# Kernel optimization log

Measured on AMD Instinct MI355X. Metric: run time of the kernel, lower is better.

## Reference

```python
import jax, jax.numpy as jnp
import numpy as np

MARGIN = 0.3

def setup_inputs() -> dict:
    key = jax.random.key(0)
    k1, k2 = jax.random.split(key)
    z1 = jax.random.normal(k1, (8192, 128), dtype=jnp.float32)
    z2 = jax.random.normal(k2, (8192, 128), dtype=jnp.float32)
    return {"z1": z1, "z2": z2}

def _cdist(z1, z2):
    # Euclidean pairwise distances via the GEMM identity, avoiding the
    # [N, N, d] broadcasted intermediate. Clamp for numerical safety.
    sq1 = jnp.sum(z1 * z1, axis=1, keepdims=True)        # [N, 1]
    sq2 = jnp.sum(z2 * z2, axis=1, keepdims=True).T      # [1, N]
    d2 = sq1 + sq2 - 2.0 * (z1 @ z2.T)                   # [N, N]
    return jnp.sqrt(jnp.maximum(d2, 0.0))

def reference(z1, z2) -> jnp.ndarray:
    n = z1.shape[0]
    dist = _cdist(z1, z2)                                # [N, N]
    pos_dist = jnp.diagonal(dist)                        # [N]
    # hard negative mining: mask diagonal with +inf, take row-min
    eye = jnp.eye(n, dtype=bool)
    neg_dist = jnp.where(eye, jnp.inf, dist)
    hard_neg = jnp.min(neg_dist, axis=1)                 # [N]
    loss = jax.nn.relu(pos_dist - hard_neg + MARGIN)
    return jnp.mean(loss)
```

## Files before the change

kernel.cpp:

```cpp
#include <hip/hip_runtime.h>

#define MARGIN 0.3f

typedef __attribute__((ext_vector_type(8))) short short8;
typedef __attribute__((ext_vector_type(4))) float floatx4;


__device__ __forceinline__ unsigned enc_f32(float f) {
    unsigned u = __float_as_uint(f);
    return (u & 0x80000000u) ? ~u : (u | 0x80000000u);
}
__device__ __forceinline__ float dec_f32(unsigned u) {
    return (u & 0x80000000u) ? __uint_as_float(u & 0x7fffffffu)
                             : __uint_as_float(~u);
}
__device__ __forceinline__ short f2bf(float f) {
    unsigned u = __float_as_uint(f);
    u = u + 0x7fffu + ((u >> 16) & 1u);
    return (short)(u >> 16);
}

__device__ __forceinline__ void gload_lds16(const void* g, void* l) {
    __builtin_amdgcn_global_load_lds(
        (const __attribute__((address_space(1))) void*)g,
        (__attribute__((address_space(3))) void*)l, 16, 0, 0);
}
__device__ __forceinline__ void gload_lds4(const void* g, void* l) {
    __builtin_amdgcn_global_load_lds(
        (const __attribute__((address_space(1))) void*)g,
        (__attribute__((address_space(3))) void*)l, 4, 0, 0);
}


__global__ void prep_kernel(const float* __restrict__ z1, const float* __restrict__ z2,
                            short* __restrict__ z1b, short* __restrict__ z2b,
                            float* __restrict__ sq1, float* __restrict__ sq2,
                            float* __restrict__ posd, unsigned* __restrict__ rowmin,
                            unsigned* __restrict__ cnt, float* __restrict__ out) {
    int h = blockIdx.x * 256 + threadIdx.x;
    int row = h >> 4, p = h & 15;
    int kk = p >> 2, q = p & 3;
    int f0 = row * 32 + kk * 8 + q * 2;
    float4 fa0 = ((const float4*)z1)[f0], fa1 = ((const float4*)z1)[f0 + 1];
    float4 fb0 = ((const float4*)z2)[f0], fb1 = ((const float4*)z2)[f0 + 1];
    short8 sa = { f2bf(fa0.x), f2bf(fa0.y), f2bf(fa0.z), f2bf(fa0.w),
                  f2bf(fa1.x), f2bf(fa1.y), f2bf(fa1.z), f2bf(fa1.w) };
    short8 sb = { f2bf(fb0.x), f2bf(fb0.y), f2bf(fb0.z), f2bf(fb0.w),
                  f2bf(fb1.x), f2bf(fb1.y), f2bf(fb1.z), f2bf(fb1.w) };
    size_t off = (size_t)(row >> 4) * 2048 + kk * 512 + q * 128 + (row & 15) * 8;
    *(short8*)&z1b[off] = sa;
    *(short8*)&z2b[off] = sb;

    float s1 = fa0.x*fa0.x + fa0.y*fa0.y + fa0.z*fa0.z + fa0.w*fa0.w
             + fa1.x*fa1.x + fa1.y*fa1.y + fa1.z*fa1.z + fa1.w*fa1.w;
    float s2 = fb0.x*fb0.x + fb0.y*fb0.y + fb0.z*fb0.z + fb0.w*fb0.w
             + fb1.x*fb1.x + fb1.y*fb1.y + fb1.z*fb1.z + fb1.w*fb1.w;
    float dx0 = fa0.x-fb0.x, dy0 = fa0.y-fb0.y, dz0 = fa0.z-fb0.z, dw0 = fa0.w-fb0.w;
    float dx1 = fa1.x-fb1.x, dy1 = fa1.y-fb1.y, dz1 = fa1.z-fb1.z, dw1 = fa1.w-fb1.w;
    float p2 = dx0*dx0 + dy0*dy0 + dz0*dz0 + dw0*dw0
             + dx1*dx1 + dy1*dy1 + dz1*dz1 + dw1*dw1;
    #pragma unroll
    for (int m = 8; m >= 1; m >>= 1) {
        s1 += __shfl_xor(s1, m);
        s2 += __shfl_xor(s2, m);
        p2 += __shfl_xor(p2, m);
    }
    if (p == 0) { sq1[row] = s1; sq2[row] = s2; posd[row] = sqrtf(p2); }

    if (threadIdx.x < 16) rowmin[blockIdx.x * 16 + threadIdx.x] = 0xFFFFFFFFu;
    if (blockIdx.x == 0) {
        if (threadIdx.x < 32) cnt[threadIdx.x] = 0u;
        if (threadIdx.x == 0) out[0] = 0.0f;
    }
}

__global__ __launch_bounds__(512, 2)
void gemm_min_kernel(const short* __restrict__ z1b, const short* __restrict__ z2b,
                     const float* __restrict__ sq1, const float* __restrict__ sq2,
                     const float* __restrict__ posd,
                     unsigned* __restrict__ rowmin, unsigned* __restrict__ cnt,
                     float* __restrict__ out, int n)
{
    __shared__ __align__(16) short sb[8][8192];
    __shared__ __align__(16) float s2l[512];
    __shared__ float lsum[8];
    __shared__ int   fin_s;

    const int bid = blockIdx.x;
    const int xcd = bid & 7, idx = bid >> 3;
    const int rg  = (xcd << 1) | (idx >> 4);
    const int cgi = idx & 15;

    const int tid = threadIdx.x, w = tid >> 6, lane = tid & 63;
    const int quad = lane >> 4, l15 = lane & 15;
    const int rowbase = rg * 512 + w * 64;
    const int colorig = cgi * 512;

    const short* gb = z2b + (size_t)(cgi * 32) * 2048;

    #pragma unroll
    for (int o = 0; o < 2; ++o)
        gload_lds16(gb + (tid + o * 512) * 8, &sb[0][(tid + o * 512) * 8]);
    __builtin_amdgcn_sched_barrier(0);
    gload_lds4(sq2 + colorig + tid, &s2l[tid]);
    __builtin_amdgcn_sched_barrier(0);

    short8 af[4][4];
    #pragma unroll
    for (int sm = 0; sm < 4; ++sm) {
        const short* pa = z1b + (size_t)(rg * 32 + w * 4 + sm) * 2048 + lane * 8;
        #pragma unroll
        for (int kk = 0; kk < 4; ++kk)
            af[sm][kk] = *(const short8*)(pa + kk * 512);
    }
    __builtin_amdgcn_sched_barrier(0);
    #pragma unroll
    for (int s = 1; s < 8; ++s) {
        #pragma unroll
        for (int o = 0; o < 2; ++o)
            gload_lds16(gb + (size_t)s * 8192 + (tid + o * 512) * 8,
                        &sb[s][(tid + o * 512) * 8]);
        __builtin_amdgcn_sched_barrier(0);
    }

    float vmin[4][4];
    #pragma unroll
    for (int sm = 0; sm < 4; ++sm)
        #pragma unroll
        for (int reg = 0; reg < 4; ++reg)
            vmin[sm][reg] = 3.0e38f;

#define SUPERPHASE(S, VMTXT)                                                   \
    do {                                                                       \
        asm volatile("s_waitcnt vmcnt(" VMTXT ")" ::: "memory");               \
        __builtin_amdgcn_sched_barrier(0);                                     \
        __builtin_amdgcn_s_barrier();                                          \
        __builtin_amdgcn_sched_barrier(0);                                     \
        const short* bs_ = &sb[S][0];                                          \
        _Pragma("unroll")                                                      \
        for (int hf = 0; hf < 2; ++hf) {                                       \
            const int tcol = (S) * 64 + hf * 32;                               \
            const int colbase = colorig + tcol;                                \
            const float s2v0 = s2l[tcol + l15];                                \
            const float s2v1 = s2l[tcol + 16 + l15];                           \
            short8 bq[2][4];                                                   \
            _Pragma("unroll")                                                  \
            for (int sn = 0; sn < 2; ++sn)                                     \
                _Pragma("unroll")                                              \
                for (int kk = 0; kk < 4; ++kk)                                 \
                    bq[sn][kk] = *(const short8*)(bs_ + hf * 4096 + sn * 2048  \
                                                  + kk * 512 + lane * 8);      \
            floatx4 acc[4][2];                                                 \
            _Pragma("unroll")                                                  \
            for (int sm = 0; sm < 4; ++sm)                                     \
                _Pragma("unroll")                                              \
                for (int sn = 0; sn < 2; ++sn)                                 \
                    acc[sm][sn] = (floatx4)0.0f;                               \
            _Pragma("unroll")                                                  \
            for (int kk = 0; kk < 4; ++kk)                                     \
                _Pragma("unroll")                                              \
                for (int sm = 0; sm < 4; ++sm)                                 \
                    _Pragma("unroll")                                          \
                    for (int sn = 0; sn < 2; ++sn)                             \
                        acc[sm][sn] = __builtin_amdgcn_mfma_f32_16x16x32_bf16( \
                            af[sm][kk], bq[sn][kk], acc[sm][sn], 0, 0, 0);     \
            if (colbase < rowbase + 64 && rowbase < colbase + 32) {            \
                _Pragma("unroll")                                              \
                for (int sm = 0; sm < 4; ++sm)                                 \
                    _Pragma("unroll")                                          \
                    for (int reg = 0; reg < 4; ++reg) {                        \
                        int gi = rowbase + sm * 16 + quad * 4 + reg;           \
                        float v0 = fmaf(-2.0f, acc[sm][0][reg], s2v0);         \
                        float v1 = fmaf(-2.0f, acc[sm][1][reg], s2v1);         \
                        v0 = (gi == colbase + l15)      ? 3.0e38f : v0;        \
                        v1 = (gi == colbase + 16 + l15) ? 3.0e38f : v1;        \
                        vmin[sm][reg] = fminf(vmin[sm][reg], fminf(v0, v1));   \
                    }                                                          \
            } else {                                                           \
                _Pragma("unroll")                                              \
                for (int sm = 0; sm < 4; ++sm)                                 \
                    _Pragma("unroll")                                          \
                    for (int reg = 0; reg < 4; ++reg) {                        \
                        float v0 = fmaf(-2.0f, acc[sm][0][reg], s2v0);         \
                        float v1 = fmaf(-2.0f, acc[sm][1][reg], s2v1);         \
                        vmin[sm][reg] = fminf(vmin[sm][reg], fminf(v0, v1));   \
                    }                                                          \
            }                                                                  \
        }                                                                      \
    } while (0)

    SUPERPHASE(0, "14");
    SUPERPHASE(1, "12");
    SUPERPHASE(2, "10");
    SUPERPHASE(3, "8");
    SUPERPHASE(4, "6");
    SUPERPHASE(5, "4");
    SUPERPHASE(6, "2");
    SUPERPHASE(7, "0");
#undef SUPERPHASE

    #pragma unroll
    for (int sm = 0; sm < 4; ++sm)
        #pragma unroll
        for (int reg = 0; reg < 4; ++reg) {
            float vm = vmin[sm][reg];
            #pragma unroll
            for (int m = 8; m >= 1; m >>= 1)
                vm = fminf(vm, __shfl_xor(vm, m));
            if (l15 == 0)
                atomicMin(&rowmin[rowbase + sm * 16 + quad * 4 + reg], enc_f32(vm));
        }

    __syncthreads();
    if (tid == 0) {
        __threadfence();
        fin_s = (atomicAdd(&cnt[rg], 1u) == 15u);
    }
    __syncthreads();
    if (!fin_s) return;
    __threadfence();

    {
        int i = rg * 512 + tid;
        unsigned rm = atomicMin(&rowmin[i], 0xFFFFFFFFu);
        float hard = sqrtf(fmaxf(sq1[i] + dec_f32(rm), 0.0f));
        float l = fmaxf(posd[i] - hard + MARGIN, 0.0f);
        #pragma unroll
        for (int m = 32; m >= 1; m >>= 1) l += __shfl_xor(l, m);
        if (lane == 0) lsum[w] = l;
    }
    __syncthreads();
    if (tid == 0) {
        float t = 0.f;
        #pragma unroll
        for (int i = 0; i < 8; ++i) t += lsum[i];
        atomicAdd(out, t / (float)n);
    }
}

extern "C" void kernel_launch(void* const* d_in, const int* in_sizes, int n_in,
                              void* d_out, int out_size, void* d_ws, size_t ws_size,
                              hipStream_t stream) {
    const float* z1 = (const float*)d_in[0];
    const float* z2 = (const float*)d_in[1];
    const int n = in_sizes[0] / 128;

    char* ws = (char*)d_ws;
    short*    z1b    = (short*)ws;
    short*    z2b    = (short*)(ws + (size_t)n * 128 * 2);
    float*    sq1    = (float*)(ws + (size_t)n * 128 * 4);
    float*    sq2    = (float*)(ws + (size_t)n * 128 * 4 + n * 4);
    float*    posd   = (float*)(ws + (size_t)n * 128 * 4 + n * 8);
    unsigned* rowmin = (unsigned*)(ws + (size_t)n * 128 * 4 + n * 12);
    unsigned* cnt    = (unsigned*)(ws + (size_t)n * 128 * 4 + n * 16);
    float*    out    = (float*)d_out;

    prep_kernel<<<n / 16, 256, 0, stream>>>(z1, z2, z1b, z2b, sq1, sq2, posd,
                                            rowmin, cnt, out);
    gemm_min_kernel<<<(n / 512) * (n / 512), 512, 0, stream>>>(
        z1b, z2b, sq1, sq2, posd, rowmin, cnt, out, n);
}
```

Measured before the change: 84.02 us.

## Fold -2 scale into bf16 z2 and seed MFMA accumulators with sq2

The prep kernel now stores z2 pre-scaled by -2 in bf16, and the GEMM accumulators are initialised with the column squared norms. The MFMA output is therefore already sq2 - 2·dot, which removes the per-element fma from the min epilogue. The change also raises wave priority around the MFMA block with s_setprio and switches the prep kernel's stores to nontemporal. Multiplying by -2 before bf16 rounding is exact, so precision is unchanged, but accumulator setup now costs register moves instead of zero initialisation.

```diff
diff --git a/kernel.cpp b/kernel.cpp
--- a/kernel.cpp
+++ b/kernel.cpp
@@ -45,11 +45,11 @@
     float4 fb0 = ((const float4*)z2)[f0], fb1 = ((const float4*)z2)[f0 + 1];
     short8 sa = { f2bf(fa0.x), f2bf(fa0.y), f2bf(fa0.z), f2bf(fa0.w),
                   f2bf(fa1.x), f2bf(fa1.y), f2bf(fa1.z), f2bf(fa1.w) };
-    short8 sb = { f2bf(fb0.x), f2bf(fb0.y), f2bf(fb0.z), f2bf(fb0.w),
-                  f2bf(fb1.x), f2bf(fb1.y), f2bf(fb1.z), f2bf(fb1.w) };
+    short8 sb = { f2bf(-2.f*fb0.x), f2bf(-2.f*fb0.y), f2bf(-2.f*fb0.z), f2bf(-2.f*fb0.w),
+                  f2bf(-2.f*fb1.x), f2bf(-2.f*fb1.y), f2bf(-2.f*fb1.z), f2bf(-2.f*fb1.w) };
     size_t off = (size_t)(row >> 4) * 2048 + kk * 512 + q * 128 + (row & 15) * 8;
-    *(short8*)&z1b[off] = sa;
-    *(short8*)&z2b[off] = sb;
+    __builtin_nontemporal_store(sa, (short8*)&z1b[off]);
+    __builtin_nontemporal_store(sb, (short8*)&z2b[off]);
 
     float s1 = fa0.x*fa0.x + fa0.y*fa0.y + fa0.z*fa0.z + fa0.w*fa0.w
              + fa1.x*fa1.x + fa1.y*fa1.y + fa1.z*fa1.z + fa1.w*fa1.w;
@@ -65,9 +65,14 @@
         s2 += __shfl_xor(s2, m);
         p2 += __shfl_xor(p2, m);
     }
-    if (p == 0) { sq1[row] = s1; sq2[row] = s2; posd[row] = sqrtf(p2); }
-
-    if (threadIdx.x < 16) rowmin[blockIdx.x * 16 + threadIdx.x] = 0xFFFFFFFFu;
+    if (p == 0) {
+        __builtin_nontemporal_store(s1, &sq1[row]);
+        __builtin_nontemporal_store(s2, &sq2[row]);
+        __builtin_nontemporal_store(sqrtf(p2), &posd[row]);
+    }
+
+    if (threadIdx.x < 16)
+        __builtin_nontemporal_store(0xFFFFFFFFu, &rowmin[blockIdx.x * 16 + threadIdx.x]);
     if (blockIdx.x == 0) {
         if (threadIdx.x < 32) cnt[threadIdx.x] = 0u;
         if (threadIdx.x == 0) out[0] = 0.0f;
@@ -152,10 +157,14 @@
                                                   + kk * 512 + lane * 8);      \
             floatx4 acc[4][2];                                                 \
             _Pragma("unroll")                                                  \
-            for (int sm = 0; sm < 4; ++sm)                                     \
-                _Pragma("unroll")                                              \
-                for (int sn = 0; sn < 2; ++sn)                                 \
-                    acc[sm][sn] = (floatx4)0.0f;                               \
+            for (int sm = 0; sm < 4; ++sm) {                                   \
+                _Pragma("unroll")                                              \
+                for (int reg = 0; reg < 4; ++reg) {                            \
+                    acc[sm][0][reg] = s2v0;                                    \
+                    acc[sm][1][reg] = s2v1;                                    \
+                }                                                              \
+            }                                                                  \
+            __builtin_amdgcn_s_setprio(1);                                     \
             _Pragma("unroll")                                                  \
             for (int kk = 0; kk < 4; ++kk)                                     \
                 _Pragma("unroll")                                              \
@@ -164,14 +173,15 @@
                     for (int sn = 0; sn < 2; ++sn)                             \
                         acc[sm][sn] = __builtin_amdgcn_mfma_f32_16x16x32_bf16( \
                             af[sm][kk], bq[sn][kk], acc[sm][sn], 0, 0, 0);     \
+            __builtin_amdgcn_s_setprio(0);                                     \
             if (colbase < rowbase + 64 && rowbase < colbase + 32) {            \
                 _Pragma("unroll")                                              \
                 for (int sm = 0; sm < 4; ++sm)                                 \
                     _Pragma("unroll")                                          \
                     for (int reg = 0; reg < 4; ++reg) {                        \
                         int gi = rowbase + sm * 16 + quad * 4 + reg;           \
-                        float v0 = fmaf(-2.0f, acc[sm][0][reg], s2v0);         \
-                        float v1 = fmaf(-2.0f, acc[sm][1][reg], s2v1);         \
+                        float v0 = acc[sm][0][reg];                            \
+                        float v1 = acc[sm][1][reg];                            \
                         v0 = (gi == colbase + l15)      ? 3.0e38f : v0;        \
                         v1 = (gi == colbase + 16 + l15) ? 3.0e38f : v1;        \
                         vmin[sm][reg] = fminf(vmin[sm][reg], fminf(v0, v1));   \
@@ -180,11 +190,9 @@
                 _Pragma("unroll")                                              \
                 for (int sm = 0; sm < 4; ++sm)                                 \
                     _Pragma("unroll")                                          \
-                    for (int reg = 0; reg < 4; ++reg) {                        \
-                        float v0 = fmaf(-2.0f, acc[sm][0][reg], s2v0);         \
-                        float v1 = fmaf(-2.0f, acc[sm][1][reg], s2v1);         \
-                        vmin[sm][reg] = fminf(vmin[sm][reg], fminf(v0, v1));   \
-                    }                                                          \
+                    for (int reg = 0; reg < 4; ++reg)                          \
+                        vmin[sm][reg] = fminf(vmin[sm][reg],                   \
+                            fminf(acc[sm][0][reg], acc[sm][1][reg]));          \
             }                                                                  \
         }                                                                      \
     } while (0)
```

Result: no change. 85.01 us (+1.2%).
